# Performance work log

Measured on AMD Instinct MI355X. Metric: run time of the kernel, lower is better.

Reference implementation:

```python
import jax, jax.numpy as jnp
import numpy as np

B, N, D, H, DK, DI = 64, 256, 1024, 8, 64, 2048
NEG = -1e9
SCALE = 1.0 / np.sqrt(DK).astype(np.float32)


def _ln(x, s, b, eps=1e-5):
    m = jnp.mean(x, axis=-1, keepdims=True)
    v = jnp.var(x, axis=-1, keepdims=True)
    return (x - m) * jax.lax.rsqrt(v + eps) * s + b


def _glat_basic(x, mask, npm, wq, wk, wv, wo, bo, ls1, lb1, w1, b1, w2, b2, ls2, lb2):
    # mask: [B,1,N,N] bool, True = blocked
    b, n, d = x.shape
    q = (x @ wq).reshape(b, n, H, DK).transpose(0, 2, 1, 3)  # [B,H,N,DK]
    k = (x @ wk).reshape(b, n, H, DK).transpose(0, 2, 1, 3)
    v = (x @ wv).reshape(b, n, H, DK).transpose(0, 2, 1, 3)
    scores = jnp.einsum('bhqd,bhkd->bhqk', q, k) * SCALE
    scores = jnp.where(mask, NEG, scores)
    attn = jax.nn.softmax(scores, axis=-1)
    out = jnp.einsum('bhqk,bhkd->bhqd', attn, v)
    out = out.transpose(0, 2, 1, 3).reshape(b, n, H * DK)
    out = out @ wo + bo
    out = _ln(out + x, ls1, lb1)           # attn residual + layernorm
    out = out * npm                         # non_pad_mask
    h = jax.nn.relu(out @ w1 + b1) @ w2 + b2
    out2 = _ln(h + out, ls2, lb2) * npm     # FFN residual + layernorm + mask
    return out2


def setup_inputs():
    key = jax.random.key(0)
    ks = jax.random.split(key, 40)
    p = lambda i, shape: jax.random.normal(ks[i], shape, jnp.float32) * 0.02
    inp = {
        'x': jax.random.normal(ks[0], (B, N, D), jnp.float32),
        'adj': jax.random.randint(ks[1], (B, N, N), 0, 2).astype(jnp.int32),
        'non_pad_mask': jnp.ones((B, N, 1), jnp.float32),
        'slf_attn_mask': jnp.zeros((B, N, N), jnp.int32),
    }
    i = 2
    for t in ('g', 'l'):
        inp[f'wq_{t}'] = p(i, (D, H * DK)); i += 1
        inp[f'wk_{t}'] = p(i, (D, H * DK)); i += 1
        inp[f'wv_{t}'] = p(i, (D, H * DK)); i += 1
        inp[f'wo_{t}'] = p(i, (H * DK, D)); i += 1
        inp[f'bo_{t}'] = jnp.zeros((D,), jnp.float32)
        inp[f'ln1s_{t}'] = jnp.ones((D,), jnp.float32)
        inp[f'ln1b_{t}'] = jnp.zeros((D,), jnp.float32)
        inp[f'w1_{t}'] = p(i, (D, DI)); i += 1
        inp[f'b1_{t}'] = jnp.zeros((DI,), jnp.float32)
        inp[f'w2_{t}'] = p(i, (DI, D)); i += 1
        inp[f'b2_{t}'] = jnp.zeros((D,), jnp.float32)
        inp[f'ln2s_{t}'] = jnp.ones((D,), jnp.float32)
        inp[f'ln2b_{t}'] = jnp.zeros((D,), jnp.float32)
    inp['fc_w'] = p(i, (2 * D, D)); i += 1
    inp['fc_b'] = jnp.zeros((D,), jnp.float32)
    return inp


def reference(x, adj, non_pad_mask, slf_attn_mask,
              wq_g, wk_g, wv_g, wo_g, bo_g, ln1s_g, ln1b_g, w1_g, b1_g, w2_g, b2_g, ln2s_g, ln2b_g,
              wq_l, wk_l, wv_l, wo_l, bo_l, ln1s_l, ln1b_l, w1_l, b1_l, w2_l, b2_l, ln2s_l, ln2b_l,
              fc_w, fc_b):
    pad_mask = (slf_attn_mask[:, None, :, :] != 0)            # [B,1,N,N]
    local_mask = pad_mask | (adj[:, None, :, :] == 0)         # local: only attend along edges
    x_g = _glat_basic(x, pad_mask, non_pad_mask,
                      wq_g, wk_g, wv_g, wo_g, bo_g, ln1s_g, ln1b_g,
                      w1_g, b1_g, w2_g, b2_g, ln2s_g, ln2b_g)
    x_l = _glat_basic(x, local_mask, non_pad_mask,
                      wq_l, wk_l, wv_l, wo_l, bo_l, ln1s_l, ln1b_l,
                      w1_l, b1_l, w2_l, b2_l, ln2s_l, ln2b_l)
    out = jnp.concatenate([x_g, x_l], axis=-1) @ fc_w + fc_b
    return out
```

## Files before the change

kernel.cpp:

```cpp
#include <hip/hip_runtime.h>


typedef unsigned short u16;
typedef unsigned long long u64;
typedef __bf16 bf16_t;
typedef bf16_t bf16x8 __attribute__((ext_vector_type(8)));
typedef float  f32x4  __attribute__((ext_vector_type(4)));
typedef u16    u16x8  __attribute__((ext_vector_type(8)));
typedef u16    u16x4  __attribute__((ext_vector_type(4)));

__device__ __forceinline__ float bf2f(u16 u){
  union { unsigned int i; float f; } c; c.i = ((unsigned int)u) << 16; return c.f;
}
__device__ __forceinline__ u16 f2bf(float f){
  union { float f; unsigned int u; } c; c.f = f;
  unsigned int u = c.u;
  unsigned int r = (u + 0x7fffu + ((u >> 16) & 1u)) >> 16;
  return (u16)r;
}

__device__ __forceinline__ void gl16(const u16* g, u16* l){
  __builtin_amdgcn_global_load_lds(
      (const __attribute__((address_space(1))) void*)g,
      (__attribute__((address_space(3))) void*)l, 16, 0, 0);
}

__global__ __launch_bounds__(256) void zero_out(float* out, int n){
  for (int i = blockIdx.x * 256 + threadIdx.x; i < n; i += 256 * 4096) out[i] = 0.f;
}

__global__ __launch_bounds__(256) void cvt_bf16(
    const float* __restrict__ in, u16* __restrict__ out)
{
  const size_t i = ((size_t)blockIdx.x * 256 + threadIdx.x) * 8;
  f32x4 a = *(const f32x4*)&in[i];
  f32x4 b = *(const f32x4*)&in[i + 4];
  u16x8 o;
  #pragma unroll
  for (int j = 0; j < 4; ++j){ o[j] = f2bf(a[j]); o[4+j] = f2bf(b[j]); }
  *(u16x8*)&out[i] = o;
}

__global__ __launch_bounds__(256) void transpose_w(
    const float* __restrict__ src, u16* __restrict__ dst, int K, int N, int dstOff)
{
  __shared__ u16 tile[32][33];
  const int bk = blockIdx.x * 32, bn = blockIdx.y * 32;
  const int t = threadIdx.x;
  const int r = t >> 5, c = t & 31;
  #pragma unroll
  for (int p = 0; p < 4; ++p)
    tile[r + p*8][c] = f2bf(src[(size_t)(bk + r + p*8) * N + bn + c]);
  __syncthreads();
  #pragma unroll
  for (int p = 0; p < 4; ++p)
    dst[(size_t)(dstOff + bn + r + p*8) * K + bk + c] = tile[c][r + p*8];
}

template<int RELU, int OF32, int ACC>
__global__ __launch_bounds__(512, 2) void gemm256(
    const u16* __restrict__ A0, const u16* __restrict__ A1,
    int Astride, int ksplit,
    const u16* __restrict__ BT, int Bld, int M, int N, int K,
    const float* __restrict__ bias, void* __restrict__ outv, int out_ld)
{
  __shared__ u16 lds[2*32768];
  const int tid  = threadIdx.x;
  const int lane = tid & 63;
  const int wid  = tid >> 6;
  const int wm = wid >> 2, wn = wid & 3;
  const int l15 = lane & 15, l4 = lane >> 4;
  const int m0 = blockIdx.x * 256, n0 = blockIdx.y * 256;

  f32x4 acc[8][4];
  #pragma unroll
  for (int i = 0; i < 8; ++i)
    #pragma unroll
    for (int j = 0; j < 4; ++j)
      acc[i][j] = (f32x4){0.f, 0.f, 0.f, 0.f};

  const int s0 = tid, s1 = tid + 512;
  const int r0 = s0 >> 3, g0 = (s0 & 7) ^ (r0 & 7);
  const int r1 = s1 >> 3, g1 = (s1 & 7) ^ (r1 & 7);

  const int nt = K >> 6;

  auto stageA = [&](int kt, int h, int buf){
    const int kb = kt * 64;
    const u16* Ab = A0; int kl = kb;
    if (kb >= ksplit){ Ab = A1; kl = kb - ksplit; }
    u16* dst = &lds[buf*32768 + h*8192];
    gl16(&Ab[(size_t)(m0 + h*128 + r0) * Astride + kl + g0*8], &dst[s0*8]);
    gl16(&Ab[(size_t)(m0 + h*128 + r1) * Astride + kl + g1*8], &dst[s1*8]);
  };
  auto stageB = [&](int kt, int h, int buf){
    const int kb = kt * 64;
    u16* dst = &lds[buf*32768 + 16384 + h*8192];
    gl16(&BT[(size_t)(n0 + h*128 + r0) * Bld + kb + g0*8], &dst[s0*8]);
    gl16(&BT[(size_t)(n0 + h*128 + r1) * Bld + kb + g1*8], &dst[s1*8]);
  };
  auto lda = [&](int i, int kc, int buf) -> bf16x8 {
    const int r = wm*128 + i*16 + l15;
    const int c = (kc*4 + l4) ^ (r & 7);
    return *(const bf16x8*)&lds[buf*32768 + r*64 + c*8];
  };
  auto ldb = [&](int j, int kc, int buf) -> bf16x8 {
    const int r = wn*64 + j*16 + l15;
    const int c = (kc*4 + l4) ^ (r & 7);
    return *(const bf16x8*)&lds[buf*32768 + 16384 + r*64 + c*8];
  };

  stageA(0, 0, 0); stageA(0, 1, 0); stageB(0, 0, 0); stageB(0, 1, 0);

  for (int t = 0; t < nt; ++t){
    const int buf = t & 1, nbuf = buf ^ 1;
    const bool pf = (t + 1 < nt);
    if (pf){
      stageA(t+1, 0, nbuf);
      asm volatile("s_waitcnt vmcnt(2)" ::: "memory");
    } else {
      asm volatile("s_waitcnt vmcnt(0)" ::: "memory");
    }
    __builtin_amdgcn_sched_barrier(0);
    __builtin_amdgcn_s_barrier();
    __builtin_amdgcn_sched_barrier(0);

    bf16x8 a_[4][2], b_[2][2];
    #pragma unroll
    for (int i = 0; i < 4; ++i){ a_[i][0] = lda(i, 0, buf); a_[i][1] = lda(i, 1, buf); }
    #pragma unroll
    for (int j = 0; j < 2; ++j){ b_[j][0] = ldb(j, 0, buf); b_[j][1] = ldb(j, 1, buf); }
    if (pf) stageA(t+1, 1, nbuf);
    __builtin_amdgcn_s_setprio(1);
    #pragma unroll
    for (int i = 0; i < 4; ++i)
      #pragma unroll
      for (int j = 0; j < 2; ++j){
        acc[i][j] = __builtin_amdgcn_mfma_f32_16x16x32_bf16(a_[i][0], b_[j][0], acc[i][j], 0,0,0);
        acc[i][j] = __builtin_amdgcn_mfma_f32_16x16x32_bf16(a_[i][1], b_[j][1], acc[i][j], 0,0,0);
      }
    __builtin_amdgcn_s_setprio(0);
    #pragma unroll
    for (int j = 0; j < 2; ++j){ b_[j][0] = ldb(2+j, 0, buf); b_[j][1] = ldb(2+j, 1, buf); }
    if (pf) stageB(t+1, 0, nbuf);
    __builtin_amdgcn_s_setprio(1);
    #pragma unroll
    for (int i = 0; i < 4; ++i)
      #pragma unroll
      for (int j = 0; j < 2; ++j){
        acc[i][2+j] = __builtin_amdgcn_mfma_f32_16x16x32_bf16(a_[i][0], b_[j][0], acc[i][2+j], 0,0,0);
        acc[i][2+j] = __builtin_amdgcn_mfma_f32_16x16x32_bf16(a_[i][1], b_[j][1], acc[i][2+j], 0,0,0);
      }
    __builtin_amdgcn_s_setprio(0);
    #pragma unroll
    for (int i = 0; i < 4; ++i){ a_[i][0] = lda(4+i, 0, buf); a_[i][1] = lda(4+i, 1, buf); }
    if (pf) stageB(t+1, 1, nbuf);
    __builtin_amdgcn_s_setprio(1);
    #pragma unroll
    for (int i = 0; i < 4; ++i)
      #pragma unroll
      for (int j = 0; j < 2; ++j){
        acc[4+i][2+j] = __builtin_amdgcn_mfma_f32_16x16x32_bf16(a_[i][0], b_[j][0], acc[4+i][2+j], 0,0,0);
        acc[4+i][2+j] = __builtin_amdgcn_mfma_f32_16x16x32_bf16(a_[i][1], b_[j][1], acc[4+i][2+j], 0,0,0);
      }
    __builtin_amdgcn_s_setprio(0);
    #pragma unroll
    for (int j = 0; j < 2; ++j){ b_[j][0] = ldb(j, 0, buf); b_[j][1] = ldb(j, 1, buf); }
    __builtin_amdgcn_s_setprio(1);
    #pragma unroll
    for (int i = 0; i < 4; ++i)
      #pragma unroll
      for (int j = 0; j < 2; ++j){
        acc[4+i][j] = __builtin_amdgcn_mfma_f32_16x16x32_bf16(a_[i][0], b_[j][0], acc[4+i][j], 0,0,0);
        acc[4+i][j] = __builtin_amdgcn_mfma_f32_16x16x32_bf16(a_[i][1], b_[j][1], acc[4+i][j], 0,0,0);
      }
    __builtin_amdgcn_s_setprio(0);

    __builtin_amdgcn_sched_barrier(0);
    __builtin_amdgcn_s_barrier();
    __builtin_amdgcn_sched_barrier(0);
  }

  const int rb = m0 + wm*128 + l4*4;
  const int cb = n0 + wn*64 + l15;
  #pragma unroll
  for (int i = 0; i < 8; ++i){
    #pragma unroll
    for (int j = 0; j < 4; ++j){
      const int col = cb + j*16;
      const float badd = bias ? bias[col] : 0.f;
      #pragma unroll
      for (int r = 0; r < 4; ++r){
        const int row = rb + i*16 + r;
        float y = acc[i][j][r] + badd;
        if (RELU) y = y > 0.f ? y : 0.f;
        if (OF32){
          float* po = &((float*)outv)[(size_t)row * out_ld + col];
          if (ACC) y += *po;
          *po = y;
        } else {
          u16* po = &((u16*)outv)[(size_t)row * out_ld + col];
          if (ACC) y += bf2f(*po);
          *po = f2bf(y);
        }
      }
    }
  }
}

__global__ __launch_bounds__(256) void mask_pack(
    const int* __restrict__ slf, const int* __restrict__ adj,
    u64* __restrict__ mb_g, u64* __restrict__ mb_l)
{
  const int idx  = blockIdx.x * 4 + (threadIdx.x >> 6);
  const int lane = threadIdx.x & 63;
  const size_t mi = (size_t)(idx >> 2) * 256 + (size_t)(idx & 3) * 64 + lane;
  const bool g = slf[mi] != 0;
  const bool l = g || (adj[mi] == 0);
  const u64 bg = __ballot(g);
  const u64 bl = __ballot(l);
  if (lane == 0){ mb_g[idx] = bg; mb_l[idx] = bl; }
}

__global__ __launch_bounds__(256) void attn_mfma(
    const u16* __restrict__ qkv, const u64* __restrict__ mb,
    int boff, u16* __restrict__ out)
{
  __shared__ u16 kbuf[64*64];
  __shared__ u16 vtbuf[64*64];
  __shared__ u16 pbuf[4][32*64];

  const int b_loc = blockIdx.x >> 4;
  const int h     = (blockIdx.x >> 1) & 7;
  const int qt    = blockIdx.x & 1;
  const int b     = boff + b_loc;
  const int t     = threadIdx.x;
  const int w     = t >> 6, lane = t & 63;
  const int l15   = lane & 15, l4 = lane >> 4;

  bf16x8 qf[2][2];
  {
    const int rbase = b_loc*256 + qt*128 + w*32;
    #pragma unroll
    for (int i = 0; i < 2; ++i)
      #pragma unroll
      for (int kc = 0; kc < 2; ++kc)
        qf[i][kc] = *(const bf16x8*)&qkv[(size_t)(rbase + i*16 + l15)*1536 + h*64 + kc*32 + l4*8];
  }

  f32x4 acc_o[2][4];
  float m_[2][4], l_[2][4];
  #pragma unroll
  for (int i = 0; i < 2; ++i){
    #pragma unroll
    for (int j = 0; j < 4; ++j) acc_o[i][j] = (f32x4){0.f,0.f,0.f,0.f};
    #pragma unroll
    for (int r = 0; r < 4; ++r){ m_[i][r] = -1e30f; l_[i][r] = 0.f; }
  }

  for (int c = 0; c < 4; ++c){
    __syncthreads();
    {
      const int kr = t >> 2, dg = (t & 3) * 16;
      const size_t rbase = (size_t)(b_loc*256 + c*64 + kr)*1536 + h*64 + dg;
      u16x8 k0 = *(const u16x8*)&qkv[rbase + 512];
      u16x8 k1 = *(const u16x8*)&qkv[rbase + 512 + 8];
      u16x8 v0 = *(const u16x8*)&qkv[rbase + 1024];
      u16x8 v1 = *(const u16x8*)&qkv[rbase + 1024 + 8];
      const int sw = (kr & 7) << 3;
      *(u16x8*)&kbuf[kr*64 + (dg ^ sw)]       = k0;
      *(u16x8*)&kbuf[kr*64 + ((dg + 8) ^ sw)] = k1;
      #pragma unroll
      for (int e = 0; e < 8; ++e){
        const int d0 = dg + e, d1 = dg + 8 + e;
        vtbuf[d0*64 + (kr ^ ((d0 & 7) << 3))] = v0[e];
        vtbuf[d1*64 + (kr ^ ((d1 & 7) << 3))] = v1[e];
      }
    }
    __syncthreads();

    bf16x8 kfr[4][2];
    #pragma unroll
    for (int jb = 0; jb < 4; ++jb){
      const int key = jb*16 + l15;
      const int sw = (key & 7) << 3;
      #pragma unroll
      for (int kc = 0; kc < 2; ++kc)
        kfr[jb][kc] = *(const bf16x8*)&kbuf[key*64 + ((kc*32 + l4*8) ^ sw)];
    }
    f32x4 s_[2][4];
    #pragma unroll
    for (int i = 0; i < 2; ++i)
      #pragma unroll
      for (int jb = 0; jb < 4; ++jb){
        f32x4 a = (f32x4){0.f,0.f,0.f,0.f};
        a = __builtin_amdgcn_mfma_f32_16x16x32_bf16(qf[i][0], kfr[jb][0], a, 0,0,0);
        a = __builtin_amdgcn_mfma_f32_16x16x32_bf16(qf[i][1], kfr[jb][1], a, 0,0,0);
        s_[i][jb] = a;
      }

    #pragma unroll
    for (int i = 0; i < 2; ++i){
      #pragma unroll
      for (int r = 0; r < 4; ++r){
        const int prow = i*16 + l4*4 + r;
        const int qrow = qt*128 + w*32 + prow;
        const u64 bits = mb[((size_t)b*256 + qrow)*4 + c];
        float sv[4];
        #pragma unroll
        for (int jb = 0; jb < 4; ++jb){
          float xv = s_[i][jb][r] * 0.125f;
          if ((bits >> (jb*16 + l15)) & 1ull) xv = -1e9f;
          sv[jb] = xv;
        }
        float mx = fmaxf(fmaxf(sv[0], sv[1]), fmaxf(sv[2], sv[3]));
        #pragma unroll
        for (int d = 1; d < 16; d <<= 1)
          mx = fmaxf(mx, __shfl_xor(mx, d, 64));
        const float mnew = fmaxf(m_[i][r], mx);
        const float corr = __expf(m_[i][r] - mnew);
        m_[i][r] = mnew;
        float ps = 0.f;
        const int swp = (prow & 7) << 3;
        #pragma unroll
        for (int jb = 0; jb < 4; ++jb){
          const float p = __expf(sv[jb] - mnew);
          ps += p;
          pbuf[w][prow*64 + ((jb*16 + l15) ^ swp)] = f2bf(p);
        }
        #pragma unroll
        for (int d = 1; d < 16; d <<= 1)
          ps += __shfl_xor(ps, d, 64);
        l_[i][r] = l_[i][r] * corr + ps;
        #pragma unroll
        for (int j2 = 0; j2 < 4; ++j2) acc_o[i][j2][r] *= corr;
      }
    }

    bf16x8 vfr[4][2];
    #pragma unroll
    for (int j2 = 0; j2 < 4; ++j2){
      const int dim = j2*16 + l15;
      const int sw = (dim & 7) << 3;
      #pragma unroll
      for (int kc = 0; kc < 2; ++kc)
        vfr[j2][kc] = *(const bf16x8*)&vtbuf[dim*64 + ((kc*32 + l4*8) ^ sw)];
    }
    #pragma unroll
    for (int i = 0; i < 2; ++i){
      const int prow = i*16 + l15;
      const int swp = (prow & 7) << 3;
      bf16x8 pa0 = *(const bf16x8*)&pbuf[w][prow*64 + ((l4*8) ^ swp)];
      bf16x8 pa1 = *(const bf16x8*)&pbuf[w][prow*64 + ((32 + l4*8) ^ swp)];
      #pragma unroll
      for (int j2 = 0; j2 < 4; ++j2){
        acc_o[i][j2] = __builtin_amdgcn_mfma_f32_16x16x32_bf16(pa0, vfr[j2][0], acc_o[i][j2], 0,0,0);
        acc_o[i][j2] = __builtin_amdgcn_mfma_f32_16x16x32_bf16(pa1, vfr[j2][1], acc_o[i][j2], 0,0,0);
      }
    }
  }

  #pragma unroll
  for (int i = 0; i < 2; ++i){
    #pragma unroll
    for (int r = 0; r < 4; ++r){
      const int qrow = qt*128 + w*32 + i*16 + l4*4 + r;
      const float inv = 1.f / l_[i][r];
      const size_t ob = ((size_t)b*256 + qrow)*512 + h*64;
      #pragma unroll
      for (int j2 = 0; j2 < 4; ++j2)
        out[ob + j2*16 + l15] = f2bf(acc_o[i][j2][r] * inv);
    }
  }
}

template<int RF32>
__global__ __launch_bounds__(256) void ln_fused(
    const u16* a, const void* __restrict__ res,
    const float* __restrict__ sc, const float* __restrict__ bs,
    const float* __restrict__ npm, u16* out)
{
  const int row = blockIdx.x, t = threadIdx.x;
  const size_t bse = (size_t)row * 1024 + t*4;
  u16x4 av = *(const u16x4*)&a[bse];
  float rv[4];
  if (RF32){
    f32x4 q = *(const f32x4*)&((const float*)res)[bse];
    #pragma unroll
    for (int j = 0; j < 4; ++j) rv[j] = q[j];
  } else {
    u16x4 q = *(const u16x4*)&((const u16*)res)[bse];
    #pragma unroll
    for (int j = 0; j < 4; ++j) rv[j] = bf2f(q[j]);
  }
  float vv[4]; float s = 0.f, sq = 0.f;
  #pragma unroll
  for (int j = 0; j < 4; ++j){
    vv[j] = bf2f(av[j]) + rv[j];
    s += vv[j]; sq += vv[j]*vv[j];
  }
  #pragma unroll
  for (int i = 1; i < 64; i <<= 1){
    s  += __shfl_xor(s,  i, 64);
    sq += __shfl_xor(sq, i, 64);
  }
  __shared__ float red[8];
  const int wid = t >> 6, lane = t & 63;
  if (lane == 0){ red[wid] = s; red[4 + wid] = sq; }
  __syncthreads();
  s  = red[0] + red[1] + red[2] + red[3];
  sq = red[4] + red[5] + red[6] + red[7];
  const float mean = s * (1.f/1024.f);
  const float var  = sq * (1.f/1024.f) - mean*mean;
  const float rstd = rsqrtf(var + 1e-5f);
  const float nm   = npm[row];
  u16x4 ov;
  #pragma unroll
  for (int j = 0; j < 4; ++j){
    float y = (vv[j] - mean) * rstd * sc[t*4+j] + bs[t*4+j];
    ov[j] = f2bf(y * nm);
  }
  *(u16x4*)&out[bse] = ov;
}

extern "C" void kernel_launch(void* const* d_in, const int* in_sizes, int n_in,
                              void* d_out, int out_size, void* d_ws, size_t ws_size,
                              hipStream_t stream)
{
  const size_t NEED = 58720256ull * 2ull;
  if (ws_size < NEED){
    zero_out<<<4096, 256, 0, stream>>>((float*)d_out, out_size);
    return;
  }

  const float* x   = (const float*)d_in[0];
  const int*   adj = (const int*)d_in[1];
  const float* npm = (const float*)d_in[2];
  const int*   slf = (const int*)d_in[3];
  const float* fcw = (const float*)d_in[30];
  const float* fcb = (const float*)d_in[31];

  u16* ws    = (u16*)d_ws;
  u16* wqkvT = ws;
  u16* woT   = ws + 1572864;
  u16* w1T   = ws + 2097152;
  u16* w2T   = ws + 4194304;
  u16* fcT   = ws + 6291456;
  u16* xbf   = ws + 8388608;
  u16* tmp   = ws + 8388608;
  u16* qkvh  = ws + 25165824;
  u16* ln1   = ws + 25165824;
  u16* xg    = ws + 41943040;

  u16* dout16 = (u16*)d_out;
  u16* attnb0 = dout16;
  u16* attnb1 = dout16 + 8388608;
  u16* hbufA  = dout16 + 16777216;
  u64* mb_g   = (u64*)(dout16 + 16777216);
  u64* mb_l   = mb_g + 65536;

  cvt_bf16<<<8192, 256, 0, stream>>>(x, xbf);
  mask_pack<<<16384, 256, 0, stream>>>(slf, adj, mb_g, mb_l);
  transpose_w<<<dim3(64, 32), 256, 0, stream>>>(fcw, fcT, 2048, 1024, 0);

  for (int L = 0; L < 2; ++L){
    const int bi = 4 + L*13;
    transpose_w<<<dim3(32, 16), 256, 0, stream>>>((const float*)d_in[bi+0], wqkvT, 1024, 512, 0);
    transpose_w<<<dim3(32, 16), 256, 0, stream>>>((const float*)d_in[bi+1], wqkvT, 1024, 512, 512);
    transpose_w<<<dim3(32, 16), 256, 0, stream>>>((const float*)d_in[bi+2], wqkvT, 1024, 512, 1024);
    u16* attnb = L ? attnb1 : attnb0;
    for (int hf = 0; hf < 2; ++hf){
      const u16* xh = xbf + (size_t)hf*8192*1024;
      gemm256<0,0,0><<<dim3(32, 6), 512, 0, stream>>>(
          xh, xh, 1024, 1024, wqkvT, 1024, 8192, 1536, 1024, nullptr, qkvh, 1536);
      attn_mfma<<<512, 256, 0, stream>>>(qkvh, L ? mb_l : mb_g, hf*32, attnb);
    }
  }

  for (int L = 0; L < 2; ++L){
    const int bi = 4 + L*13;
    const float* bo  = (const float*)d_in[bi+4];
    const float* l1s = (const float*)d_in[bi+5];
    const float* l1b = (const float*)d_in[bi+6];
    const float* b1  = (const float*)d_in[bi+8];
    const float* b2  = (const float*)d_in[bi+10];
    const float* l2s = (const float*)d_in[bi+11];
    const float* l2b = (const float*)d_in[bi+12];

    transpose_w<<<dim3(16, 32), 256, 0, stream>>>((const float*)d_in[bi+3], woT, 512, 1024, 0);
    transpose_w<<<dim3(32, 64), 256, 0, stream>>>((const float*)d_in[bi+7], w1T, 1024, 2048, 0);
    transpose_w<<<dim3(64, 32), 256, 0, stream>>>((const float*)d_in[bi+9], w2T, 2048, 1024, 0);

    const u16* attnb = L ? attnb1 : attnb0;
    gemm256<0,0,0><<<dim3(64, 4), 512, 0, stream>>>(
        attnb, attnb, 512, 512, woT, 512, 16384, 1024, 512, bo, tmp, 1024);
    ln_fused<1><<<16384, 256, 0, stream>>>(tmp, x, l1s, l1b, npm, ln1);
    for (int hh = 0; hh < 2; ++hh){
      gemm256<1,0,0><<<dim3(64, 4), 512, 0, stream>>>(
          ln1, ln1, 1024, 1024, w1T + (size_t)hh*1024*1024, 1024,
          16384, 1024, 1024, b1 + hh*1024, hbufA, 1024);
      if (hh == 0)
        gemm256<0,0,0><<<dim3(64, 4), 512, 0, stream>>>(
            hbufA, hbufA, 1024, 1024, w2T, 2048, 16384, 1024, 1024, b2, tmp, 1024);
      else
        gemm256<0,0,1><<<dim3(64, 4), 512, 0, stream>>>(
            hbufA, hbufA, 1024, 1024, w2T + 1024, 2048, 16384, 1024, 1024,
            nullptr, tmp, 1024);
    }
    ln_fused<0><<<16384, 256, 0, stream>>>(tmp, ln1, l2s, l2b, npm, L ? tmp : xg);
  }

  gemm256<0,1,0><<<dim3(64, 4), 512, 0, stream>>>(
      xg, tmp, 1024, 1024, fcT, 2048, 16384, 1024, 2048, fcb, d_out, 1024);
}
```

Baseline: 805.2 us.

## Restructure GEMM main loop, remap workgroups across XCDs, merge QKV weight transposes

The GEMM main loop now issues all next-tile global-to-LDS loads at the top of each iteration and waits with vmcnt(8). The MFMA work is reorganized into two larger phases that hold all four B fragments in registers at once. Workgroup indices are permuted in groups of eight so consecutive tiles map to the same XCD, aiming for better L2 reuse. The three per-layer QKV weight transpose launches are merged into one 3D-grid launch to cut launch overhead. In exchange, register pressure rises and the finer interleaving of loads with MFMAs is lost.

```diff
diff --git a/kernel.cpp b/kernel.cpp
--- a/kernel.cpp
+++ b/kernel.cpp
@@ -57,6 +57,25 @@
     dst[(size_t)(dstOff + bn + r + p*8) * K + bk + c] = tile[c][r + p*8];
 }
 
+__global__ __launch_bounds__(256) void transpose_w3(
+    const float* __restrict__ sA, const float* __restrict__ sB,
+    const float* __restrict__ sC, u16* __restrict__ dst, int K, int N)
+{
+  __shared__ u16 tile[32][33];
+  const float* src = blockIdx.z == 0 ? sA : (blockIdx.z == 1 ? sB : sC);
+  const int dstOff = blockIdx.z * N;
+  const int bk = blockIdx.x * 32, bn = blockIdx.y * 32;
+  const int t = threadIdx.x;
+  const int r = t >> 5, c = t & 31;
+  #pragma unroll
+  for (int p = 0; p < 4; ++p)
+    tile[r + p*8][c] = f2bf(src[(size_t)(bk + r + p*8) * N + bn + c]);
+  __syncthreads();
+  #pragma unroll
+  for (int p = 0; p < 4; ++p)
+    dst[(size_t)(dstOff + bn + r + p*8) * K + bk + c] = tile[c][r + p*8];
+}
+
 template<int RELU, int OF32, int ACC>
 __global__ __launch_bounds__(512, 2) void gemm256(
     const u16* __restrict__ A0, const u16* __restrict__ A1,
@@ -70,7 +89,13 @@
   const int wid  = tid >> 6;
   const int wm = wid >> 2, wn = wid & 3;
   const int l15 = lane & 15, l4 = lane >> 4;
-  const int m0 = blockIdx.x * 256, n0 = blockIdx.y * 256;
+
+  const int gx = gridDim.x;
+  int lin = blockIdx.y * gx + blockIdx.x;
+  const int nwg = gx * gridDim.y;
+  if ((nwg & 7) == 0)
+    lin = (lin & 7) * (nwg >> 3) + (lin >> 3);
+  const int m0 = (lin % gx) * 256, n0 = (lin / gx) * 256;
 
   f32x4 acc[8][4];
   #pragma unroll
@@ -114,10 +139,10 @@
 
   for (int t = 0; t < nt; ++t){
     const int buf = t & 1, nbuf = buf ^ 1;
-    const bool pf = (t + 1 < nt);
-    if (pf){
-      stageA(t+1, 0, nbuf);
-      asm volatile("s_waitcnt vmcnt(2)" ::: "memory");
+    if (t + 1 < nt){
+      stageA(t+1, 0, nbuf); stageA(t+1, 1, nbuf);
+      stageB(t+1, 0, nbuf); stageB(t+1, 1, nbuf);
+      asm volatile("s_waitcnt vmcnt(8)" ::: "memory");
     } else {
       asm volatile("s_waitcnt vmcnt(0)" ::: "memory");
     }
@@ -125,52 +150,27 @@
     __builtin_amdgcn_s_barrier();
     __builtin_amdgcn_sched_barrier(0);
 
-    bf16x8 a_[4][2], b_[2][2];
+    bf16x8 a_[4][2], b_[4][2];
+    #pragma unroll
+    for (int j = 0; j < 4; ++j){ b_[j][0] = ldb(j, 0, buf); b_[j][1] = ldb(j, 1, buf); }
     #pragma unroll
     for (int i = 0; i < 4; ++i){ a_[i][0] = lda(i, 0, buf); a_[i][1] = lda(i, 1, buf); }
-    #pragma unroll
-    for (int j = 0; j < 2; ++j){ b_[j][0] = ldb(j, 0, buf); b_[j][1] = ldb(j, 1, buf); }
-    if (pf) stageA(t+1, 1, nbuf);
     __builtin_amdgcn_s_setprio(1);
     #pragma unroll
     for (int i = 0; i < 4; ++i)
       #pragma unroll
-      for (int j = 0; j < 2; ++j){
+      for (int j = 0; j < 4; ++j){
         acc[i][j] = __builtin_amdgcn_mfma_f32_16x16x32_bf16(a_[i][0], b_[j][0], acc[i][j], 0,0,0);
         acc[i][j] = __builtin_amdgcn_mfma_f32_16x16x32_bf16(a_[i][1], b_[j][1], acc[i][j], 0,0,0);
       }
     __builtin_amdgcn_s_setprio(0);
     #pragma unroll
-    for (int j = 0; j < 2; ++j){ b_[j][0] = ldb(2+j, 0, buf); b_[j][1] = ldb(2+j, 1, buf); }
-    if (pf) stageB(t+1, 0, nbuf);
+    for (int i = 0; i < 4; ++i){ a_[i][0] = lda(4+i, 0, buf); a_[i][1] = lda(4+i, 1, buf); }
     __builtin_amdgcn_s_setprio(1);
     #pragma unroll
     for (int i = 0; i < 4; ++i)
       #pragma unroll
-      for (int j = 0; j < 2; ++j){
-        acc[i][2+j] = __builtin_amdgcn_mfma_f32_16x16x32_bf16(a_[i][0], b_[j][0], acc[i][2+j], 0,0,0);
-        acc[i][2+j] = __builtin_amdgcn_mfma_f32_16x16x32_bf16(a_[i][1], b_[j][1], acc[i][2+j], 0,0,0);
-      }
-    __builtin_amdgcn_s_setprio(0);
-    #pragma unroll
-    for (int i = 0; i < 4; ++i){ a_[i][0] = lda(4+i, 0, buf); a_[i][1] = lda(4+i, 1, buf); }
-    if (pf) stageB(t+1, 1, nbuf);
-    __builtin_amdgcn_s_setprio(1);
-    #pragma unroll
-    for (int i = 0; i < 4; ++i)
-      #pragma unroll
-      for (int j = 0; j < 2; ++j){
-        acc[4+i][2+j] = __builtin_amdgcn_mfma_f32_16x16x32_bf16(a_[i][0], b_[j][0], acc[4+i][2+j], 0,0,0);
-        acc[4+i][2+j] = __builtin_amdgcn_mfma_f32_16x16x32_bf16(a_[i][1], b_[j][1], acc[4+i][2+j], 0,0,0);
-      }
-    __builtin_amdgcn_s_setprio(0);
-    #pragma unroll
-    for (int j = 0; j < 2; ++j){ b_[j][0] = ldb(j, 0, buf); b_[j][1] = ldb(j, 1, buf); }
-    __builtin_amdgcn_s_setprio(1);
-    #pragma unroll
-    for (int i = 0; i < 4; ++i)
-      #pragma unroll
-      for (int j = 0; j < 2; ++j){
+      for (int j = 0; j < 4; ++j){
         acc[4+i][j] = __builtin_amdgcn_mfma_f32_16x16x32_bf16(a_[i][0], b_[j][0], acc[4+i][j], 0,0,0);
         acc[4+i][j] = __builtin_amdgcn_mfma_f32_16x16x32_bf16(a_[i][1], b_[j][1], acc[4+i][j], 0,0,0);
       }
@@ -465,9 +465,9 @@
 
   for (int L = 0; L < 2; ++L){
     const int bi = 4 + L*13;
-    transpose_w<<<dim3(32, 16), 256, 0, stream>>>((const float*)d_in[bi+0], wqkvT, 1024, 512, 0);
-    transpose_w<<<dim3(32, 16), 256, 0, stream>>>((const float*)d_in[bi+1], wqkvT, 1024, 512, 512);
-    transpose_w<<<dim3(32, 16), 256, 0, stream>>>((const float*)d_in[bi+2], wqkvT, 1024, 512, 1024);
+    transpose_w3<<<dim3(32, 16, 3), 256, 0, stream>>>(
+        (const float*)d_in[bi+0], (const float*)d_in[bi+1],
+        (const float*)d_in[bi+2], wqkvT, 1024, 512);
     u16* attnb = L ? attnb1 : attnb0;
     for (int hf = 0; hf < 2; ++hf){
       const u16* xh = xbf + (size_t)hf*8192*1024;
```

After: 862.0 us. +7.1%, slower.
